# Kernel optimization log

Hardware: AMD Instinct MI355X
Metric: run time of the kernel (lower is better)

## Reference

```python
import jax, jax.numpy as jnp
import numpy as np
import math

TOPK = 13
NUM_CLASSES = 80
ALPHA = 1.0
BETA = 6.0
EPS = 1e-9


def setup_inputs() -> dict:
    key = jax.random.key(0)
    ks = jax.random.split(key, 7)
    bs, na, nc, ng = 16, 8400, 80, 128
    pd_scores = jax.random.uniform(ks[0], (bs, na, nc), dtype=jnp.float32)
    # valid xyxy predicted boxes: center in [0,640], w/h in [8,72]
    pc = jax.random.uniform(ks[1], (bs, na, 2), dtype=jnp.float32) * 640.0
    pwh = jax.random.uniform(ks[2], (bs, na, 2), dtype=jnp.float32) * 64.0 + 8.0
    pd_bboxes = jnp.concatenate([pc - pwh / 2, pc + pwh / 2], axis=-1)
    anc_points = jax.random.uniform(ks[3], (na, 2), dtype=jnp.float32) * 640.0
    gt_labels = jax.random.randint(ks[4], (bs, ng, 1), 0, nc, dtype=jnp.int64)
    gc = jax.random.uniform(ks[5], (bs, ng, 2), dtype=jnp.float32) * 640.0
    gwh = jax.random.uniform(ks[6], (bs, ng, 2), dtype=jnp.float32) * 128.0 + 16.0
    gt_bboxes = jnp.concatenate([gc - gwh / 2, gc + gwh / 2], axis=-1)
    gt_mask = jnp.ones((bs, ng, 1), dtype=jnp.float32)
    return {"pd_scores": pd_scores, "pd_bboxes": pd_bboxes, "anc_points": anc_points,
            "gt_labels": gt_labels, "gt_bboxes": gt_bboxes, "gt_mask": gt_mask}


def _ciou(b1, b2, eps=1e-7):
    # b1: (bs, na, 1, 4), b2: (bs, 1, ng, 4), xyxy format -> CIoU (bs, na, ng)
    b1x1, b1y1, b1x2, b1y2 = b1[..., 0], b1[..., 1], b1[..., 2], b1[..., 3]
    b2x1, b2y1, b2x2, b2y2 = b2[..., 0], b2[..., 1], b2[..., 2], b2[..., 3]
    inter = jnp.clip(jnp.minimum(b1x2, b2x2) - jnp.maximum(b1x1, b2x1), 0) * \
            jnp.clip(jnp.minimum(b1y2, b2y2) - jnp.maximum(b1y1, b2y1), 0)
    w1, h1 = b1x2 - b1x1, b1y2 - b1y1 + eps
    w2, h2 = b2x2 - b2x1, b2y2 - b2y1 + eps
    union = w1 * h1 + w2 * h2 - inter + eps
    iou = inter / union
    cw = jnp.maximum(b1x2, b2x2) - jnp.minimum(b1x1, b2x1)
    ch = jnp.maximum(b1y2, b2y2) - jnp.minimum(b1y1, b2y1)
    c2 = cw * cw + ch * ch + eps
    rho2 = ((b2x1 + b2x2 - b1x1 - b1x2) ** 2 + (b2y1 + b2y2 - b1y1 - b1y2) ** 2) / 4.0
    v = (4.0 / math.pi ** 2) * (jnp.arctan(w2 / h2) - jnp.arctan(w1 / h1)) ** 2
    alpha = jax.lax.stop_gradient(v / (v - iou + (1.0 + eps)))
    return iou - (rho2 / c2 + v * alpha)


def reference(pd_scores, pd_bboxes, anc_points, gt_labels, gt_bboxes, gt_mask):
    bs, na, nc = pd_scores.shape
    ng = gt_bboxes.shape[1]
    gt_m = gt_mask[..., 0]  # (bs, ng) float

    # --- anchors whose center lies inside each GT box: (bs, na, ng) ---
    lt = gt_bboxes[:, None, :, :2]                    # (bs, 1, ng, 2)
    rb = gt_bboxes[:, None, :, 2:]
    anc = anc_points[None, :, None, :]                # (1, na, 1, 2)
    deltas = jnp.concatenate([anc - lt, rb - anc], axis=-1)  # (bs, na, ng, 4)
    mask_in_gts = (deltas.min(axis=-1) > EPS)         # (bs, na, ng) bool
    mask_pos = mask_in_gts.astype(pd_scores.dtype) * gt_m[:, None, :]

    # --- alignment metric: score^alpha * CIoU^beta, masked ---
    iou = jnp.clip(_ciou(pd_bboxes[:, :, None, :], gt_bboxes[:, None, :, :]), 0.0)
    gl = gt_labels[..., 0].astype(jnp.int32)          # (bs, ng)
    idx = jnp.broadcast_to(gl[:, None, :], (bs, na, ng))
    target_scores_g = jnp.take_along_axis(pd_scores, idx, axis=2)  # (bs, na, ng)
    align = (target_scores_g ** ALPHA) * (iou ** BETA) * mask_pos

    # --- per-GT top-k anchors, scattered into (bs, na, ng) 0/1 mask ---
    mt = jnp.swapaxes(align, 1, 2)                    # (bs, ng, na)
    _, top_idx = jax.lax.top_k(mt, TOPK)              # (bs, ng, TOPK)
    bi = jnp.arange(bs)[:, None, None]
    gi = jnp.arange(ng)[None, :, None]
    is_in = jnp.zeros((bs, ng, na), jnp.int32).at[bi, gi, top_idx].set(1)
    is_in = jnp.swapaxes(is_in, 1, 2)                 # (bs, na, ng)
    is_in = is_in * (gt_m[:, None, :] > 0).astype(jnp.int32)
    is_in = jnp.where(align > 1e-9, is_in, 0)

    # --- conflict resolution (faithful to module's arithmetic) ---
    conflict = is_in.sum(axis=-1) > 1                 # (bs, na)
    best_gt = jnp.argmax(align, axis=-1)              # (bs, na)
    one_hot_best = jax.nn.one_hot(best_gt, ng, dtype=jnp.int32)
    keep = (~conflict)[..., None].astype(jnp.int32)
    resolved = is_in * keep + one_hot_best * keep
    is_in = jnp.where(conflict.any(), resolved, is_in)

    final_mask = is_in.sum(axis=-1) > 0               # (bs, na) bool
    target_gt_idx = jnp.argmax(is_in, axis=-1)        # (bs, na)

    # --- gather targets ---
    flat = jnp.arange(bs)[:, None] * ng + target_gt_idx
    target_cls = gl.reshape(-1)[flat]                 # (bs, na)
    target_bboxes = gt_bboxes.reshape(-1, 4)[flat]    # (bs, na, 4)
    target_scores = jax.nn.one_hot(target_cls, NUM_CLASSES, dtype=pd_scores.dtype)

    # --- normalized alignment ---
    is_in_f = is_in.astype(align.dtype)
    amf = align * is_in_f
    max_metrics = amf.max(axis=-1, keepdims=True)
    max_iou = (iou * is_in_f).max(axis=-1, keepdims=True)
    norm_align = (max_metrics * amf / (max_iou + 1e-9)).max(axis=-1, keepdims=True)
    target_scores = target_scores * norm_align
    return (target_cls, target_bboxes, target_scores, final_mask, norm_align)
```

## Files before the change

### kernel.cpp

```cpp
#include <hip/hip_runtime.h>
#include <math.h>

#pragma clang fp contract(off)

#define BS 16
#define NA 8400
#define NG 128
#define NC 80
#define KTOP 13
#define QCAP 1024
#define NCH (QCAP / 64)

#define OFF_BITS   0
#define OFF_SELCNT ((size_t)BS * NA * 16)
#define OFF_FLAG   (OFF_SELCNT + (size_t)BS * NA * 4)
#define OFF_BESTK  (OFF_FLAG + 256)

#define OUT_CLS    0
#define OUT_BBOX   (BS * NA)
#define OUT_SCORES (OUT_BBOX + BS * NA * 4)
#define OUT_MASK   (OUT_SCORES + BS * NA * NC)
#define OUT_NORM   (OUT_MASK + BS * NA)

__device__ __forceinline__ float dev_ciou(float px1, float py1, float px2, float py2,
                                          float gx1, float gy1, float gx2, float gy2) {
    const float eps = 1e-7f;
    float iw = fminf(px2, gx2) - fmaxf(px1, gx1); iw = fmaxf(iw, 0.0f);
    float ih = fminf(py2, gy2) - fmaxf(py1, gy1); ih = fmaxf(ih, 0.0f);
    float inter = iw * ih;
    float w1 = px2 - px1;
    float h1 = (py2 - py1) + eps;
    float w2 = gx2 - gx1;
    float h2 = (gy2 - gy1) + eps;
    float uni = ((w1 * h1 + w2 * h2) - inter) + eps;
    float iou = inter / uni;
    float cw = fmaxf(px2, gx2) - fminf(px1, gx1);
    float ch = fmaxf(py2, gy2) - fminf(py1, gy1);
    float c2 = (cw * cw + ch * ch) + eps;
    float tx = ((gx1 + gx2) - px1) - px2;
    float ty = ((gy1 + gy2) - py1) - py2;
    float rho2 = (tx * tx + ty * ty) / 4.0f;
    float da = atanf(w2 / h2) - atanf(w1 / h1);
    float v = ((float)(4.0 / (M_PI * M_PI))) * (da * da);
    float alpha = v / ((v - iou) + (float)(1.0 + 1e-7));
    float res = iou - (rho2 / c2 + v * alpha);
    return fmaxf(res, 0.0f);
}

__global__ __launch_bounds__(256) void k_init(
    unsigned int* __restrict__ bits, unsigned int* __restrict__ selcnt,
    int* __restrict__ flag, unsigned long long* __restrict__ bestkey)
{
    int i = blockIdx.x * 256 + threadIdx.x;
    if (i < BS * NA) {
        ((uint4*)bits)[i] = make_uint4(0u, 0u, 0u, 0u);
        selcnt[i] = 0u;
        bestkey[i] = 127ULL;
    }
    if (i == 0) *flag = 0;
}

__global__ __launch_bounds__(256) void k_build_select(
    const float* __restrict__ scores, const float* __restrict__ pboxes,
    const float* __restrict__ anc, const int* __restrict__ glab,
    const float* __restrict__ gboxes, const float* __restrict__ gmask,
    unsigned int* __restrict__ bits, unsigned int* __restrict__ selcnt,
    int* __restrict__ flag, unsigned long long* __restrict__ bestkey)
{
    __shared__ unsigned short s_idx[QCAP];
    __shared__ float s_val[QCAP];
    __shared__ unsigned int s_qn;

    int g = blockIdx.x, b = blockIdx.y;
    int col = b * NG + g;
    int tid = threadIdx.x;
    float gm = gmask[col];
    float gx1 = gboxes[col * 4 + 0], gy1 = gboxes[col * 4 + 1];
    float gx2 = gboxes[col * 4 + 2], gy2 = gboxes[col * 4 + 3];
    int cls = glab[col];
    if (tid == 0) s_qn = 0;
    __syncthreads();

    if (gm != 0.0f) {
        for (int a = tid; a < NA; a += 256) {
            float2 ap = ((const float2*)anc)[a];
            float mn = fminf(fminf(ap.x - gx1, ap.y - gy1), fminf(gx2 - ap.x, gy2 - ap.y));
            if (mn > 1e-9f) {
                unsigned int pos = atomicAdd(&s_qn, 1u);
                if (pos < QCAP) s_idx[pos] = (unsigned short)a;
            }
        }
    }
    __syncthreads();
    int qn = (int)s_qn; if (qn > QCAP) qn = QCAP;

    for (int i = tid; i < qn; i += 256) {
        int a = (int)s_idx[i];
        size_t t = (size_t)b * NA + a;
        float4 pb = ((const float4*)pboxes)[t];
        float iou = dev_ciou(pb.x, pb.y, pb.z, pb.w, gx1, gy1, gx2, gy2);
        float s = scores[t * NC + cls];
        float al = (s * powf(iou, 6.0f)) * gm;
        s_val[i] = (al > 1e-9f) ? al : -1.0f;
        unsigned long long key =
            ((unsigned long long)__float_as_uint(al) << 32) | (unsigned int)(127 - g);
        atomicMax(&bestkey[t], key);
    }
    __syncthreads();

    if (!(gm > 0.0f)) return;
    if (tid >= 64) return;
    int lane = tid;
    float v[NCH]; unsigned int ai[NCH];
    int nch = (qn + 63) >> 6;
    #pragma unroll
    for (int j = 0; j < NCH; j++) {
        int i = j * 64 + lane;
        if (i < qn) { v[j] = s_val[i]; ai[j] = (unsigned int)s_idx[i]; }
        else        { v[j] = -1.0f;    ai[j] = 0xFFFFFFFFu; }
    }
    for (int k = 0; k < KTOP; k++) {
        float bv = -1.0f; unsigned int ba = 0xFFFFFFFFu;
        #pragma unroll
        for (int j = 0; j < NCH; j++) {
            if (j < nch) {
                if (v[j] > bv || (v[j] == bv && ai[j] < ba)) { bv = v[j]; ba = ai[j]; }
            }
        }
        for (int off = 1; off < 64; off <<= 1) {
            float ov = __shfl_xor(bv, off);
            unsigned int oa = (unsigned int)__shfl_xor((int)ba, off);
            if (ov > bv || (ov == bv && oa < ba)) { bv = ov; ba = oa; }
        }
        if (!(bv > 1e-9f)) break;
        #pragma unroll
        for (int j = 0; j < NCH; j++) {
            if (ai[j] == ba) v[j] = -1.0f;
        }
        if (lane == 0) {
            size_t t = (size_t)b * NA + ba;
            atomicOr(&bits[t * 4 + (g >> 5)], 1u << (g & 31));
            unsigned int old = atomicAdd(&selcnt[t], 1u);
            if (old >= 1u) atomicOr(flag, 1);
        }
    }
}

__global__ __launch_bounds__(256) void k_final(
    const float* __restrict__ scores, const float* __restrict__ pboxes,
    const int* __restrict__ glab, const float* __restrict__ gboxes,
    const float* __restrict__ gmask,
    const unsigned int* __restrict__ bits, const int* __restrict__ flagp,
    const unsigned long long* __restrict__ bestkey,
    float* __restrict__ o_cls, float* __restrict__ o_bbox, float* __restrict__ o_scores,
    float* __restrict__ o_mask, float* __restrict__ o_norm)
{
    __shared__ float4 s_gb[NG];
    __shared__ int s_gl[NG];
    __shared__ float s_gm[NG];
    int b = blockIdx.y;
    for (int i = threadIdx.x; i < NG; i += 256) {
        s_gb[i] = ((const float4*)gboxes)[b * NG + i];
        s_gl[i] = glab[b * NG + i];
        s_gm[i] = gmask[b * NG + i];
    }
    __syncthreads();
    int a = blockIdx.x * 256 + threadIdx.x;
    if (a >= NA) return;
    size_t t = (size_t)b * NA + a;
    unsigned int ew[4];
    ew[0] = bits[t * 4 + 0]; ew[1] = bits[t * 4 + 1];
    ew[2] = bits[t * 4 + 2]; ew[3] = bits[t * 4 + 3];
    int cnt = __popc(ew[0]) + __popc(ew[1]) + __popc(ew[2]) + __popc(ew[3]);
    bool conflict_any = (flagp[0] != 0);
    unsigned long long key = bestkey[t];
    float best_v = __uint_as_float((unsigned int)(key >> 32));
    int best_g = 127 - (int)(key & 0x7Fu);
    float4 pb = ((const float4*)pboxes)[t];
    const float* srow = scores + t * NC;

    bool keep = (cnt <= 1);
    float M = 0.0f, mxiou = 0.0f;
    int tgt = 0;
    float fmask = 0.0f;

    if (!conflict_any) {
        fmask = (cnt > 0) ? 1.0f : 0.0f;
        for (int w = 0; w < 4; w++) {
            if (ew[w]) { tgt = w * 32 + __ffs(ew[w]) - 1; break; }
        }
        for (int w = 0; w < 4; w++) {
            unsigned int m = ew[w];
            while (m) {
                int j = __ffs(m) - 1; m &= m - 1;
                int g = w * 32 + j;
                float4 gb = s_gb[g];
                float iv = dev_ciou(pb.x, pb.y, pb.z, pb.w, gb.x, gb.y, gb.z, gb.w);
                float s = srow[s_gl[g]];
                float av = (s * powf(iv, 6.0f)) * s_gm[g];
                M = fmaxf(M, av);
                mxiou = fmaxf(mxiou, iv);
            }
        }
    } else if (!keep) {
        fmask = 0.0f; tgt = 0; M = 0.0f; mxiou = 0.0f;
    } else {
        fmask = 1.0f;
        bool eff_best = ((ew[best_g >> 5] >> (best_g & 31)) & 1u) != 0u;
        int first_eff = 1 << 30;
        for (int w = 0; w < 4; w++) {
            if (ew[w]) { first_eff = w * 32 + __ffs(ew[w]) - 1; break; }
        }
        tgt = eff_best ? best_g : (first_eff < best_g ? first_eff : best_g);
        for (int w = 0; w < 4; w++) {
            unsigned int m = ew[w];
            while (m) {
                int j = __ffs(m) - 1; m &= m - 1;
                int g = w * 32 + j;
                float r = (g == best_g) ? 2.0f : 1.0f;
                float4 gb = s_gb[g];
                float iv = dev_ciou(pb.x, pb.y, pb.z, pb.w, gb.x, gb.y, gb.z, gb.w);
                float s = srow[s_gl[g]];
                float av = (s * powf(iv, 6.0f)) * s_gm[g];
                M = fmaxf(M, av * r);
                mxiou = fmaxf(mxiou, iv * r);
            }
        }
        if (!eff_best) {
            float4 gb = s_gb[best_g];
            float iv = dev_ciou(pb.x, pb.y, pb.z, pb.w, gb.x, gb.y, gb.z, gb.w);
            M = fmaxf(M, best_v);
            mxiou = fmaxf(mxiou, iv);
        }
    }

    float norm = (M * M) / (mxiou + 1e-9f);
    int cls = s_gl[tgt];
    float4 gb = s_gb[tgt];
    o_cls[t] = (float)cls;
    ((float4*)o_bbox)[t] = gb;
    o_mask[t] = fmask;
    o_norm[t] = norm;
    float* orow = o_scores + t * (size_t)NC;
    #pragma unroll
    for (int j = 0; j < NC / 4; j++) {
        int base = j * 4;
        float4 z;
        z.x = (cls == base + 0) ? norm : 0.0f;
        z.y = (cls == base + 1) ? norm : 0.0f;
        z.z = (cls == base + 2) ? norm : 0.0f;
        z.w = (cls == base + 3) ? norm : 0.0f;
        ((float4*)orow)[j] = z;
    }
}

extern "C" void kernel_launch(void* const* d_in, const int* in_sizes, int n_in,
                              void* d_out, int out_size, void* d_ws, size_t ws_size,
                              hipStream_t stream) {
    const float* pd_scores = (const float*)d_in[0];
    const float* pd_bboxes = (const float*)d_in[1];
    const float* anc       = (const float*)d_in[2];
    const int*   glab      = (const int*)d_in[3];
    const float* gboxes    = (const float*)d_in[4];
    const float* gmask     = (const float*)d_in[5];
    float* out = (float*)d_out;

    char* ws = (char*)d_ws;
    unsigned int*       bits    = (unsigned int*)(ws + OFF_BITS);
    unsigned int*       selcnt  = (unsigned int*)(ws + OFF_SELCNT);
    int*                flag    = (int*)(ws + OFF_FLAG);
    unsigned long long* bestkey = (unsigned long long*)(ws + OFF_BESTK);

    k_init<<<(BS * NA + 255) / 256, 256, 0, stream>>>(bits, selcnt, flag, bestkey);

    k_build_select<<<dim3(NG, BS), 256, 0, stream>>>(
        pd_scores, pd_bboxes, anc, glab, gboxes, gmask, bits, selcnt, flag, bestkey);

    k_final<<<dim3((NA + 255) / 256, BS), 256, 0, stream>>>(
        pd_scores, pd_bboxes, glab, gboxes, gmask, bits, flag, bestkey,
        out + OUT_CLS, out + OUT_BBOX, out + OUT_SCORES, out + OUT_MASK, out + OUT_NORM);
}
```

Before: 145.7 us.

## Map one wavefront per GT box with ballot compaction and shared-memory top-k

Reorganizes the build/select kernel so each 64-lane wavefront handles one ground-truth box instead of a whole 256-thread block per box. Candidate anchors are compacted with ballot/popcount in anchor order rather than shared atomics, which removes block barriers and leaves the other three waves no longer idle during top-k. Top-k now scans shared memory per iteration instead of holding 16-chunk register arrays, and the global atomics are issued in one batch afterwards. The trade-off is that each wave scans all anchors alone, and every top-k pass re-reads the shared-memory candidate list.

```diff
diff --git a/kernel.cpp b/kernel.cpp
--- a/kernel.cpp
+++ b/kernel.cpp
@@ -9,7 +9,6 @@
 #define NC 80
 #define KTOP 13
 #define QCAP 1024
-#define NCH (QCAP / 64)
 
 #define OFF_BITS   0
 #define OFF_SELCNT ((size_t)BS * NA * 16)
@@ -67,82 +66,97 @@
     unsigned int* __restrict__ bits, unsigned int* __restrict__ selcnt,
     int* __restrict__ flag, unsigned long long* __restrict__ bestkey)
 {
-    __shared__ unsigned short s_idx[QCAP];
-    __shared__ float s_val[QCAP];
-    __shared__ unsigned int s_qn;
-
-    int g = blockIdx.x, b = blockIdx.y;
-    int col = b * NG + g;
-    int tid = threadIdx.x;
+    __shared__ unsigned short s_idx[4][QCAP];
+    __shared__ float s_val[4][QCAP];
+    int wv = threadIdx.x >> 6, lane = threadIdx.x & 63;
+    int col = blockIdx.x * 4 + wv;
+    int b = col >> 7, g = col & 127;
     float gm = gmask[col];
+    if (gm == 0.0f) return;
     float gx1 = gboxes[col * 4 + 0], gy1 = gboxes[col * 4 + 1];
     float gx2 = gboxes[col * 4 + 2], gy2 = gboxes[col * 4 + 3];
     int cls = glab[col];
-    if (tid == 0) s_qn = 0;
-    __syncthreads();
-
-    if (gm != 0.0f) {
-        for (int a = tid; a < NA; a += 256) {
-            float2 ap = ((const float2*)anc)[a];
-            float mn = fminf(fminf(ap.x - gx1, ap.y - gy1), fminf(gx2 - ap.x, gy2 - ap.y));
-            if (mn > 1e-9f) {
-                unsigned int pos = atomicAdd(&s_qn, 1u);
-                if (pos < QCAP) s_idx[pos] = (unsigned short)a;
-            }
-        }
-    }
-    __syncthreads();
-    int qn = (int)s_qn; if (qn > QCAP) qn = QCAP;
-
-    for (int i = tid; i < qn; i += 256) {
-        int a = (int)s_idx[i];
+    unsigned short* qi = s_idx[wv];
+    float* qv = s_val[wv];
+    unsigned long long lmask = (1ULL << lane) - 1ULL;
+
+    int qn = 0;
+    #pragma unroll 4
+    for (int base = 0; base < NA / 2; base += 64) {
+        int p = base + lane;
+        bool h0 = false, h1 = false;
+        int a0 = 2 * p, a1 = 2 * p + 1;
+        if (p < NA / 2) {
+            float4 ap = ((const float4*)anc)[p];
+            float m0 = fminf(fminf(ap.x - gx1, ap.y - gy1), fminf(gx2 - ap.x, gy2 - ap.y));
+            float m1 = fminf(fminf(ap.z - gx1, ap.w - gy1), fminf(gx2 - ap.z, gy2 - ap.w));
+            h0 = (m0 > 1e-9f);
+            h1 = (m1 > 1e-9f);
+        }
+        unsigned long long b0 = __ballot(h0);
+        unsigned long long b1 = __ballot(h1);
+        int c0 = __popcll(b0);
+        if (h0) {
+            int pos = qn + __popcll(b0 & lmask);
+            if (pos < QCAP) qi[pos] = (unsigned short)a0;
+        }
+        if (h1) {
+            int pos = qn + c0 + __popcll(b1 & lmask);
+            if (pos < QCAP) qi[pos] = (unsigned short)a1;
+        }
+        qn += c0 + __popcll(b1);
+    }
+    if (qn > QCAP) qn = QCAP;
+
+    for (int i = lane; i < qn; i += 64) {
+        int a = (int)qi[i];
         size_t t = (size_t)b * NA + a;
         float4 pb = ((const float4*)pboxes)[t];
         float iou = dev_ciou(pb.x, pb.y, pb.z, pb.w, gx1, gy1, gx2, gy2);
         float s = scores[t * NC + cls];
         float al = (s * powf(iou, 6.0f)) * gm;
-        s_val[i] = (al > 1e-9f) ? al : -1.0f;
+        qv[i] = (al > 1e-9f) ? al : -1.0f;
         unsigned long long key =
             ((unsigned long long)__float_as_uint(al) << 32) | (unsigned int)(127 - g);
         atomicMax(&bestkey[t], key);
     }
-    __syncthreads();
 
     if (!(gm > 0.0f)) return;
-    if (tid >= 64) return;
-    int lane = tid;
-    float v[NCH]; unsigned int ai[NCH];
-    int nch = (qn + 63) >> 6;
+    unsigned int wins[KTOP];
+    int nw = 0;
     #pragma unroll
-    for (int j = 0; j < NCH; j++) {
-        int i = j * 64 + lane;
-        if (i < qn) { v[j] = s_val[i]; ai[j] = (unsigned int)s_idx[i]; }
-        else        { v[j] = -1.0f;    ai[j] = 0xFFFFFFFFu; }
-    }
     for (int k = 0; k < KTOP; k++) {
-        float bv = -1.0f; unsigned int ba = 0xFFFFFFFFu;
-        #pragma unroll
-        for (int j = 0; j < NCH; j++) {
-            if (j < nch) {
-                if (v[j] > bv || (v[j] == bv && ai[j] < ba)) { bv = v[j]; ba = ai[j]; }
-            }
-        }
+        float bv = -1.0f; unsigned int ba = 0xFFFFFFFFu; int bp = -1;
+        for (int i = lane; i < qn; i += 64) {
+            float v = qv[i]; unsigned int a = qi[i];
+            if (v > bv || (v == bv && a < ba)) { bv = v; ba = a; bp = i; }
+        }
+        float mybv = bv; unsigned int myba = ba; int mybp = bp;
         for (int off = 1; off < 64; off <<= 1) {
             float ov = __shfl_xor(bv, off);
             unsigned int oa = (unsigned int)__shfl_xor((int)ba, off);
             if (ov > bv || (ov == bv && oa < ba)) { bv = ov; ba = oa; }
         }
         if (!(bv > 1e-9f)) break;
+        wins[k] = ba; nw = k + 1;
+        if (myba == ba && mybv == bv && mybp >= 0) qv[mybp] = -1.0f;
+    }
+    if (lane == 0 && nw > 0) {
+        unsigned int olds[KTOP];
         #pragma unroll
-        for (int j = 0; j < NCH; j++) {
-            if (ai[j] == ba) v[j] = -1.0f;
-        }
-        if (lane == 0) {
-            size_t t = (size_t)b * NA + ba;
-            atomicOr(&bits[t * 4 + (g >> 5)], 1u << (g & 31));
-            unsigned int old = atomicAdd(&selcnt[t], 1u);
-            if (old >= 1u) atomicOr(flag, 1);
-        }
+        for (int k = 0; k < KTOP; k++) {
+            if (k < nw) {
+                size_t t = (size_t)b * NA + wins[k];
+                atomicOr(&bits[t * 4 + (g >> 5)], 1u << (g & 31));
+                olds[k] = atomicAdd(&selcnt[t], 1u);
+            }
+        }
+        bool c = false;
+        #pragma unroll
+        for (int k = 0; k < KTOP; k++) {
+            if (k < nw && olds[k] >= 1u) c = true;
+        }
+        if (c) atomicOr(flag, 1);
     }
 }
 
@@ -273,7 +287,7 @@
 
     k_init<<<(BS * NA + 255) / 256, 256, 0, stream>>>(bits, selcnt, flag, bestkey);
 
-    k_build_select<<<dim3(NG, BS), 256, 0, stream>>>(
+    k_build_select<<<dim3(BS * NG / 4), 256, 0, stream>>>(
         pd_scores, pd_bboxes, anc, glab, gboxes, gmask, bits, selcnt, flag, bestkey);
 
     k_final<<<dim3((NA + 255) / 256, BS), 256, 0, stream>>>(
```

Measured after the change: 158.9 us. 1.09x slower.
